# Performance work log

Hardware: AMD Instinct MI355X
Metric: run time of the kernel (lower is better)

## Reference

```python
import jax, jax.numpy as jnp
import numpy as np

B, S, D_MODEL = 2, 2048, 2048
N_HEADS, D_HEAD = 32, 64
SEQ_MAX = 2048


def _rope_cache(seq_len, d_head):
    half = d_head // 2
    inv_freq = 1.0 / (10000.0 ** (np.arange(0, half, dtype=np.float32) / half))
    t = np.arange(seq_len, dtype=np.float32)
    freqs = np.einsum('i,j->ij', t, inv_freq)  # [S, half]
    emb = np.concatenate([freqs, freqs], axis=-1)  # [S, d_head]
    return jnp.asarray(np.cos(emb)), jnp.asarray(np.sin(emb))


def _rotate_half(x):
    half = x.shape[-1] // 2
    return jnp.concatenate([-x[..., half:], x[..., :half]], axis=-1)


def setup_inputs() -> dict:
    key = jax.random.key(0)
    ks = jax.random.split(key, 9)
    std = 0.02
    mk = lambda k: jax.random.normal(k, (D_MODEL, D_MODEL), jnp.float32) * std
    return {
        'x': jax.random.normal(ks[0], (B, S, D_MODEL), jnp.float32),
        'Wq': mk(ks[1]), 'bq': jnp.zeros((D_MODEL,), jnp.float32),
        'Wk': mk(ks[2]), 'bk': jnp.zeros((D_MODEL,), jnp.float32),
        'Wv': mk(ks[3]), 'bv': jnp.zeros((D_MODEL,), jnp.float32),
        'Wo': mk(ks[4]), 'bo': jnp.zeros((D_MODEL,), jnp.float32),
    }


def reference(x, Wq, bq, Wk, bk, Wv, bv, Wo, bo):
    Bsz, S_len, _ = x.shape
    # projections (torch Linear: y = x @ W^T + b)
    q = x @ Wq.T + bq
    k = x @ Wk.T + bk
    v = x @ Wv.T + bv
    # [B, H, S, Dh]
    to_heads = lambda t: t.reshape(Bsz, S_len, N_HEADS, D_HEAD).transpose(0, 2, 1, 3)
    q, k, v = to_heads(q), to_heads(k), to_heads(v)
    cos, sin = _rope_cache(S_len, D_HEAD)  # [S, Dh]
    cos = cos[None, None]
    sin = sin[None, None]
    q = q * cos + _rotate_half(q) * sin
    k = k * cos + _rotate_half(k) * sin
    scale = 1.0 / jnp.sqrt(jnp.float32(D_HEAD))
    att = jnp.einsum('bhqd,bhkd->bhqk', q, k) * scale
    causal = jnp.tril(jnp.ones((S_len, S_len), dtype=bool))
    att = jnp.where(causal[None, None], att, jnp.float32(-jnp.inf))
    att = jax.nn.softmax(att, axis=-1)
    # sigmoid-gated values (dropout = identity at inference)
    y = jnp.einsum('bhqk,bhkd->bhqd', att, jax.nn.sigmoid(v))
    y = y.transpose(0, 2, 1, 3).reshape(Bsz, S_len, D_MODEL)
    return y @ Wo.T + bo
```

## Files before the change

kernel.cpp:

```cpp
#include <hip/hip_runtime.h>

typedef unsigned short u16;
typedef float f32x4 __attribute__((ext_vector_type(4)));
typedef __bf16 bf16x8 __attribute__((ext_vector_type(8)));

#define S_LEN 2048
#define DM 2048
#define NHEAD 32
#define DHEAD 64

__device__ __forceinline__ u16 f2bf(float f) {
    __bf16 b = (__bf16)f;
    return __builtin_bit_cast(u16, b);
}
__device__ __forceinline__ float bf2f(u16 u) {
    return (float)__builtin_bit_cast(__bf16, u);
}
__device__ __forceinline__ void async16(const void* g, void* l) {
    __builtin_amdgcn_global_load_lds(
        (const __attribute__((address_space(1))) unsigned int*)g,
        (__attribute__((address_space(3))) unsigned int*)l, 16, 0, 0);
}
__device__ __forceinline__ void fast_sincos(float th, float* s, float* c) {
    float rev = th * 0.15915494309189535f;
    rev = rev - floorf(rev);
    *s = __builtin_amdgcn_sinf(rev);
    *c = __builtin_amdgcn_cosf(rev);
}
__device__ __forceinline__ float fexp2(float x) { return __builtin_amdgcn_exp2f(x); }

__global__ __launch_bounds__(256) void cast_all(const float* __restrict__ x,
                                                const float* __restrict__ Wq,
                                                const float* __restrict__ Wk,
                                                const float* __restrict__ Wv,
                                                const float* __restrict__ Wo,
                                                u16* __restrict__ xb,
                                                u16* __restrict__ Wqkv,
                                                u16* __restrict__ Wob) {
    int bid = blockIdx.x;
    const float* src;
    u16* dst;
    long long off;
    if (bid < 8192)       { src = x;  dst = xb;             off = (long long)bid * 1024; }
    else if (bid < 12288) { src = Wq; dst = Wqkv;           off = (long long)(bid - 8192) * 1024; }
    else if (bid < 16384) { src = Wk; dst = Wqkv + 4194304; off = (long long)(bid - 12288) * 1024; }
    else if (bid < 20480) { src = Wv; dst = Wqkv + 8388608; off = (long long)(bid - 16384) * 1024; }
    else                  { src = Wo; dst = Wob;            off = (long long)(bid - 20480) * 1024; }
    long long i = off + threadIdx.x * 4;
    float4 f = *(const float4*)(src + i);
    ushort4 v;
    v.x = f2bf(f.x); v.y = f2bf(f.y); v.z = f2bf(f.z); v.w = f2bf(f.w);
    *(ushort4*)(dst + i) = v;
}

__global__ __launch_bounds__(256) void rope_qk(u16* __restrict__ Qb, u16* __restrict__ Kb) {
    long long idx = (long long)blockIdx.x * 256 + threadIdx.x;
    int which = (int)(idx >> 22);
    int t = (int)(idx & 4194303);
    int j = t & 31;
    int h = (t >> 5) & 31;
    int row = t >> 10;
    int s = row & (S_LEN - 1);
    u16* T = which ? Kb : Qb;
    float scale = which ? 1.0f : 0.18033688011112042f;
    long long base = (long long)row * DM + h * DHEAD;
    float inv = __expf(-(float)j * 0.28782313662425575f);
    float sn, cs;
    fast_sincos((float)s * inv, &sn, &cs);
    float x1 = bf2f(T[base + j]);
    float x2 = bf2f(T[base + 32 + j]);
    T[base + j] = f2bf((x1 * cs - x2 * sn) * scale);
    T[base + 32 + j] = f2bf((x2 * cs + x1 * sn) * scale);
}

__global__ __launch_bounds__(256) void gemm_qkv(const u16* __restrict__ A,
                                                const u16* __restrict__ Bt,
                                                const float* __restrict__ bq,
                                                const float* __restrict__ bk,
                                                const float* __restrict__ bv,
                                                u16* __restrict__ Qo, u16* __restrict__ Ko,
                                                u16* __restrict__ VTo, int M, int K) {
    __shared__ __align__(16) u16 As[128 * 32];
    __shared__ __align__(16) u16 Bs[128 * 32];
    int tid = threadIdx.x;
    int w = tid >> 6, lane = tid & 63, quad = lane >> 4, l16 = lane & 15;
    int m0 = blockIdx.x * 128;
    int n0 = blockIdx.y * 128;
    int sel = n0 >> 11;
    int nloc = n0 & 2047;
    int wm = (w & 1) * 64, wn = (w >> 1) * 64;

    f32x4 acc[4][4] = {};
    const u16* ga = A + (long long)m0 * K;
    const u16* gb = Bt + (long long)n0 * K;

    for (int k0 = 0; k0 < K; k0 += 32) {
#pragma unroll
        for (int rr = 0; rr < 2; ++rr) {
            int c = tid + rr * 256;
            int row = c >> 2, kc = c & 3;
            async16(ga + (long long)row * K + k0 + kc * 8, (char*)As + c * 16);
            async16(gb + (long long)row * K + k0 + kc * 8, (char*)Bs + c * 16);
        }
        __syncthreads();
        bf16x8 af[4], bfv[4];
#pragma unroll
        for (int mt = 0; mt < 4; ++mt)
            af[mt] = *(const bf16x8*)(As + (wm + mt * 16 + l16) * 32 + quad * 8);
#pragma unroll
        for (int nt = 0; nt < 4; ++nt)
            bfv[nt] = *(const bf16x8*)(Bs + (wn + nt * 16 + l16) * 32 + quad * 8);
#pragma unroll
        for (int mt = 0; mt < 4; ++mt)
#pragma unroll
            for (int nt = 0; nt < 4; ++nt)
                acc[mt][nt] = __builtin_amdgcn_mfma_f32_16x16x32_bf16(af[mt], bfv[nt],
                                                                      acc[mt][nt], 0, 0, 0);
        __syncthreads();
    }

    if (sel < 2) {
        u16* out = sel == 0 ? Qo : Ko;
        const float* bias = sel == 0 ? bq : bk;
#pragma unroll
        for (int mt = 0; mt < 4; ++mt) {
#pragma unroll
            for (int nt = 0; nt < 4; ++nt) {
                int col = nloc + wn + nt * 16 + l16;
                float bvs = bias[col];
#pragma unroll
                for (int r = 0; r < 4; ++r) {
                    int row = m0 + wm + mt * 16 + quad * 4 + r;
                    out[(long long)row * 2048 + col] = f2bf(acc[mt][nt][r] + bvs);
                }
            }
        }
    } else {
#pragma unroll
        for (int mt = 0; mt < 4; ++mt) {
            int rowb = m0 + wm + mt * 16 + quad * 4;
            int b = rowb >> 11;
            int s0 = rowb & (S_LEN - 1);
#pragma unroll
            for (int nt = 0; nt < 4; ++nt) {
                int col = nloc + wn + nt * 16 + l16;
                int h = col >> 6, d = col & 63;
                float bvs = bv[col];
                ushort4 pk;
                pk.x = f2bf(1.f / (1.f + __expf(-(acc[mt][nt][0] + bvs))));
                pk.y = f2bf(1.f / (1.f + __expf(-(acc[mt][nt][1] + bvs))));
                pk.z = f2bf(1.f / (1.f + __expf(-(acc[mt][nt][2] + bvs))));
                pk.w = f2bf(1.f / (1.f + __expf(-(acc[mt][nt][3] + bvs))));
                *(ushort4*)(VTo + ((long long)((b * NHEAD + h) * DHEAD + d)) * S_LEN + s0) = pk;
            }
        }
    }
}

__global__ __launch_bounds__(256) void gemm_bt_f32(const u16* __restrict__ A,
                                                   const u16* __restrict__ Bt,
                                                   const float* __restrict__ bias,
                                                   float* __restrict__ Cout,
                                                   int M, int N, int K) {
    __shared__ __align__(16) u16 As[128 * 32];
    __shared__ __align__(16) u16 Bs[128 * 32];
    int tid = threadIdx.x;
    int w = tid >> 6, lane = tid & 63, quad = lane >> 4, l16 = lane & 15;
    int m0 = blockIdx.x * 128;
    int n0 = blockIdx.y * 128;
    int wm = (w & 1) * 64, wn = (w >> 1) * 64;

    f32x4 acc[4][4] = {};
    const u16* ga = A + (long long)m0 * K;
    const u16* gb = Bt + (long long)n0 * K;

    for (int k0 = 0; k0 < K; k0 += 32) {
#pragma unroll
        for (int rr = 0; rr < 2; ++rr) {
            int c = tid + rr * 256;
            int row = c >> 2, kc = c & 3;
            async16(ga + (long long)row * K + k0 + kc * 8, (char*)As + c * 16);
            async16(gb + (long long)row * K + k0 + kc * 8, (char*)Bs + c * 16);
        }
        __syncthreads();
        bf16x8 af[4], bfv[4];
#pragma unroll
        for (int mt = 0; mt < 4; ++mt)
            af[mt] = *(const bf16x8*)(As + (wm + mt * 16 + l16) * 32 + quad * 8);
#pragma unroll
        for (int nt = 0; nt < 4; ++nt)
            bfv[nt] = *(const bf16x8*)(Bs + (wn + nt * 16 + l16) * 32 + quad * 8);
#pragma unroll
        for (int mt = 0; mt < 4; ++mt)
#pragma unroll
            for (int nt = 0; nt < 4; ++nt)
                acc[mt][nt] = __builtin_amdgcn_mfma_f32_16x16x32_bf16(af[mt], bfv[nt],
                                                                      acc[mt][nt], 0, 0, 0);
        __syncthreads();
    }

#pragma unroll
    for (int mt = 0; mt < 4; ++mt) {
#pragma unroll
        for (int nt = 0; nt < 4; ++nt) {
            int col = n0 + wn + nt * 16 + l16;
            float bvs = bias[col];
#pragma unroll
            for (int r = 0; r < 4; ++r) {
                int row = m0 + wm + mt * 16 + quad * 4 + r;
                Cout[(long long)row * N + col] = acc[mt][nt][r] + bvs;
            }
        }
    }
}

__global__ __launch_bounds__(256, 2) void flash_attn(const u16* __restrict__ Q,
                                                     const u16* __restrict__ K,
                                                     const u16* __restrict__ VT,
                                                     u16* __restrict__ Y) {
    int bid = blockIdx.x;
    int pi = bid & 7;
    int h = (bid >> 3) & 31;
    int b = bid >> 8;
    int tid = threadIdx.x;
    int w = tid >> 6, lane = tid & 63, quad = lane >> 4, l16 = lane & 15;

    __shared__ __align__(16) u16 Kl[2][64 * 64];
    __shared__ __align__(16) u16 Vl[2][64 * 64];
    __shared__ __align__(16) u16 Pl[4][32 * 64];

    const u16* kbase = K + ((long long)(b * S_LEN)) * DM + h * DHEAD;
    const u16* vbase = VT + ((long long)((b * NHEAD + h) * DHEAD)) * S_LEN;

    bf16x8 kpre[2], vpre[2];
    int c0 = tid, c1 = tid + 256;
    int row0 = c0 >> 3, lc0 = (c0 & 7) ^ (row0 & 7);
    int row1 = c1 >> 3, lc1 = (c1 & 7) ^ (row1 & 7);

    kpre[0] = *(const bf16x8*)(kbase + (long long)row0 * DM + lc0 * 8);
    vpre[0] = *(const bf16x8*)(vbase + (long long)row0 * S_LEN + lc0 * 8);
    kpre[1] = *(const bf16x8*)(kbase + (long long)row1 * DM + lc1 * 8);
    vpre[1] = *(const bf16x8*)(vbase + (long long)row1 * S_LEN + lc1 * 8);

    int it = 0;
#pragma unroll 1
    for (int rep = 0; rep < 2; ++rep) {
        int qt = rep ? 15 - pi : pi;
        bf16x8 aq[2][2];
#pragma unroll
        for (int sub = 0; sub < 2; ++sub) {
            int qrow = qt * 128 + w * 32 + sub * 16 + l16;
            const u16* qp = Q + ((long long)(b * S_LEN + qrow)) * DM + h * DHEAD + quad * 8;
            aq[sub][0] = *(const bf16x8*)(qp);
            aq[sub][1] = *(const bf16x8*)(qp + 32);
        }

        f32x4 o[2][4] = {};
        float m_r[2] = {-__builtin_inff(), -__builtin_inff()};
        float l_r[2] = {0.f, 0.f};

        int kts = 2 * qt + 2;
#pragma unroll 1
        for (int kt = 0; kt < kts; ++kt) {
            u16* Kb_ = Kl[it & 1];
            u16* Vb_ = Vl[it & 1];
            *(bf16x8*)((char*)Kb_ + c0 * 16) = kpre[0];
            *(bf16x8*)((char*)Vb_ + c0 * 16) = vpre[0];
            *(bf16x8*)((char*)Kb_ + c1 * 16) = kpre[1];
            *(bf16x8*)((char*)Vb_ + c1 * 16) = vpre[1];
            {
                int nk0 = (kt + 1 < kts ? kt + 1 : 0) * 64;
                kpre[0] = *(const bf16x8*)(kbase + (long long)(nk0 + row0) * DM + lc0 * 8);
                vpre[0] = *(const bf16x8*)(vbase + (long long)row0 * S_LEN + nk0 + lc0 * 8);
                kpre[1] = *(const bf16x8*)(kbase + (long long)(nk0 + row1) * DM + lc1 * 8);
                vpre[1] = *(const bf16x8*)(vbase + (long long)row1 * S_LEN + nk0 + lc1 * 8);
            }
            __syncthreads();

            bf16x8 ak0[4], ak1[4];
#pragma unroll
            for (int nt = 0; nt < 4; ++nt) {
                int row = nt * 16 + l16;
                ak0[nt] = *(const bf16x8*)(Kb_ + row * 64 + (quad ^ (row & 7)) * 8);
                ak1[nt] = *(const bf16x8*)(Kb_ + row * 64 + ((quad + 4) ^ (row & 7)) * 8);
            }

            bf16x8 bp[2][2];
            u16* pw = &Pl[w][0];
#pragma unroll
            for (int sub = 0; sub < 2; ++sub) {
                f32x4 s[4];
#pragma unroll
                for (int nt = 0; nt < 4; ++nt) {
                    f32x4 a = {};
                    a = __builtin_amdgcn_mfma_f32_16x16x32_bf16(ak0[nt], aq[sub][0], a, 0, 0, 0);
                    a = __builtin_amdgcn_mfma_f32_16x16x32_bf16(ak1[nt], aq[sub][1], a, 0, 0, 0);
                    s[nt] = a;
                }
                if (kt >= 2 * qt) {
                    int qg = qt * 128 + w * 32 + sub * 16 + l16;
#pragma unroll
                    for (int nt = 0; nt < 4; ++nt) {
#pragma unroll
                        for (int r = 0; r < 4; ++r) {
                            int kg = kt * 64 + nt * 16 + quad * 4 + r;
                            if (kg > qg) s[nt][r] = -__builtin_inff();
                        }
                    }
                }
                float mx = s[0][0];
#pragma unroll
                for (int nt = 0; nt < 4; ++nt)
#pragma unroll
                    for (int r = 0; r < 4; ++r) mx = fmaxf(mx, s[nt][r]);
                mx = fmaxf(mx, __shfl_xor(mx, 16, 64));
                mx = fmaxf(mx, __shfl_xor(mx, 32, 64));
                float mnew = fmaxf(m_r[sub], mx);
                float alpha = fexp2(m_r[sub] - mnew);
                m_r[sub] = mnew;
#pragma unroll
                for (int nt = 0; nt < 4; ++nt)
#pragma unroll
                    for (int r = 0; r < 4; ++r) s[nt][r] = fexp2(s[nt][r] - mnew);
                float sum = 0.f;
#pragma unroll
                for (int nt = 0; nt < 4; ++nt)
#pragma unroll
                    for (int r = 0; r < 4; ++r) sum += s[nt][r];
                sum += __shfl_xor(sum, 16, 64);
                sum += __shfl_xor(sum, 32, 64);
                l_r[sub] = l_r[sub] * alpha + sum;
#pragma unroll
                for (int dt = 0; dt < 4; ++dt)
#pragma unroll
                    for (int r = 0; r < 4; ++r) o[sub][dt][r] *= alpha;

                int prow = sub * 16 + l16;
#pragma unroll
                for (int nt = 0; nt < 4; ++nt) {
                    ushort4 pk;
                    pk.x = f2bf(s[nt][0]); pk.y = f2bf(s[nt][1]);
                    pk.z = f2bf(s[nt][2]); pk.w = f2bf(s[nt][3]);
                    int chunk = (nt * 2 + (quad >> 1)) ^ (l16 & 7);
                    *(ushort4*)(pw + prow * 64 + chunk * 8 + (quad & 1) * 4) = pk;
                }
                bp[sub][0] = *(const bf16x8*)(pw + prow * 64 + (quad ^ (l16 & 7)) * 8);
                bp[sub][1] = *(const bf16x8*)(pw + prow * 64 + ((quad + 4) ^ (l16 & 7)) * 8);
            }

#pragma unroll
            for (int dt = 0; dt < 4; ++dt) {
                int row = dt * 16 + l16;
                bf16x8 av0 = *(const bf16x8*)(Vb_ + row * 64 + (quad ^ (row & 7)) * 8);
                bf16x8 av1 = *(const bf16x8*)(Vb_ + row * 64 + ((quad + 4) ^ (row & 7)) * 8);
#pragma unroll
                for (int sub = 0; sub < 2; ++sub) {
                    o[sub][dt] = __builtin_amdgcn_mfma_f32_16x16x32_bf16(av0, bp[sub][0],
                                                                         o[sub][dt], 0, 0, 0);
                    o[sub][dt] = __builtin_amdgcn_mfma_f32_16x16x32_bf16(av1, bp[sub][1],
                                                                         o[sub][dt], 0, 0, 0);
                }
            }
            ++it;
        }

#pragma unroll
        for (int sub = 0; sub < 2; ++sub) {
            float inv_l = 1.f / l_r[sub];
            u16* yp = Y + ((long long)(b * S_LEN + qt * 128 + w * 32 + sub * 16 + l16)) * DM
                      + h * DHEAD;
#pragma unroll
            for (int dt = 0; dt < 4; ++dt) {
                ushort4 yk;
                yk.x = f2bf(o[sub][dt][0] * inv_l);
                yk.y = f2bf(o[sub][dt][1] * inv_l);
                yk.z = f2bf(o[sub][dt][2] * inv_l);
                yk.w = f2bf(o[sub][dt][3] * inv_l);
                *(ushort4*)(yp + dt * 16 + quad * 4) = yk;
            }
        }
    }
}

extern "C" void kernel_launch(void* const* d_in, const int* in_sizes, int n_in,
                              void* d_out, int out_size, void* d_ws, size_t ws_size,
                              hipStream_t stream) {
    const float* x  = (const float*)d_in[0];
    const float* Wq = (const float*)d_in[1];
    const float* bq = (const float*)d_in[2];
    const float* Wk = (const float*)d_in[3];
    const float* bk = (const float*)d_in[4];
    const float* Wv = (const float*)d_in[5];
    const float* bv = (const float*)d_in[6];
    const float* Wo = (const float*)d_in[7];
    const float* bo = (const float*)d_in[8];

    const long long M = 2LL * S_LEN;

    char* ws = (char*)d_ws;
    u16* xb   = (u16*)(ws);
    u16* Wqkv = (u16*)(ws + 16 * 1024 * 1024);
    u16* Wob  = (u16*)(ws + 40 * 1024 * 1024);
    u16* Qb   = (u16*)(ws + 48 * 1024 * 1024);
    u16* Kb   = (u16*)(ws + 64 * 1024 * 1024);
    u16* VTb  = (u16*)(ws + 80 * 1024 * 1024);
    u16* Yb   = (u16*)(ws + 96 * 1024 * 1024);

    cast_all<<<24576, 256, 0, stream>>>(x, Wq, Wk, Wv, Wo, xb, Wqkv, Wob);

    dim3 gqkv(32, 48);
    gemm_qkv<<<gqkv, 256, 0, stream>>>(xb, Wqkv, bq, bk, bv, Qb, Kb, VTb, (int)M, DM);

    rope_qk<<<32768, 256, 0, stream>>>(Qb, Kb);

    flash_attn<<<2 * NHEAD * 8, 256, 0, stream>>>(Qb, Kb, VTb, Yb);

    dim3 gg(32, 16);
    gemm_bt_f32<<<gg, 256, 0, stream>>>(Yb, Wob, bo, (float*)d_out, (int)M, DM, DM);
}
```

Before: 431.1 us.

## Move V sigmoid and transpose into RoPE kernel; remap attention blocks per XCD

The QKV GEMM epilogue no longer writes V with a strided, scattered transpose. It now writes V row-major like Q and K, and a new branch in the RoPE kernel applies the sigmoid and transposes 64x64 tiles through shared memory into the VT layout. The flash attention block index is also remapped so that blocks sharing a head land on the same XCD, which should improve L2 reuse of K and V. The cost is an extra write and read pass over V plus a larger workspace.

```diff
diff --git a/kernel.cpp b/kernel.cpp
--- a/kernel.cpp
+++ b/kernel.cpp
@@ -53,24 +53,53 @@
     *(ushort4*)(dst + i) = v;
 }
 
-__global__ __launch_bounds__(256) void rope_qk(u16* __restrict__ Qb, u16* __restrict__ Kb) {
-    long long idx = (long long)blockIdx.x * 256 + threadIdx.x;
-    int which = (int)(idx >> 22);
-    int t = (int)(idx & 4194303);
-    int j = t & 31;
-    int h = (t >> 5) & 31;
-    int row = t >> 10;
-    int s = row & (S_LEN - 1);
-    u16* T = which ? Kb : Qb;
-    float scale = which ? 1.0f : 0.18033688011112042f;
-    long long base = (long long)row * DM + h * DHEAD;
-    float inv = __expf(-(float)j * 0.28782313662425575f);
-    float sn, cs;
-    fast_sincos((float)s * inv, &sn, &cs);
-    float x1 = bf2f(T[base + j]);
-    float x2 = bf2f(T[base + 32 + j]);
-    T[base + j] = f2bf((x1 * cs - x2 * sn) * scale);
-    T[base + 32 + j] = f2bf((x2 * cs + x1 * sn) * scale);
+__global__ __launch_bounds__(256) void rope_vsig(u16* __restrict__ Qb, u16* __restrict__ Kb,
+                                                 const u16* __restrict__ V,
+                                                 u16* __restrict__ VT) {
+    int bid = blockIdx.x;
+    if (bid < 32768) {
+        long long idx = (long long)bid * 256 + threadIdx.x;
+        int which = (int)(idx >> 22);
+        int t = (int)(idx & 4194303);
+        int j = t & 31;
+        int h = (t >> 5) & 31;
+        int row = t >> 10;
+        int s = row & (S_LEN - 1);
+        u16* T = which ? Kb : Qb;
+        float scale = which ? 1.0f : 0.18033688011112042f;
+        long long base = (long long)row * DM + h * DHEAD;
+        float inv = __expf(-(float)j * 0.28782313662425575f);
+        float sn, cs;
+        fast_sincos((float)s * inv, &sn, &cs);
+        float x1 = bf2f(T[base + j]);
+        float x2 = bf2f(T[base + 32 + j]);
+        T[base + j] = f2bf((x1 * cs - x2 * sn) * scale);
+        T[base + 32 + j] = f2bf((x2 * cs + x1 * sn) * scale);
+    } else {
+        int vb = bid - 32768;
+        int st = vb & 63;
+        int h = vb >> 6;
+        __shared__ u16 T[64][72];
+        int r = threadIdx.x >> 2, c0 = (threadIdx.x & 3) * 16;
+        const u16* src = V + (long long)(st * 64 + r) * DM + h * 64 + c0;
+#pragma unroll
+        for (int half = 0; half < 2; ++half) {
+            bf16x8 v = *(const bf16x8*)(src + half * 8);
+#pragma unroll
+            for (int j = 0; j < 8; ++j) {
+                float vf = (float)v[j];
+                T[c0 + half * 8 + j][r] = f2bf(1.f / (1.f + __expf(-vf)));
+            }
+        }
+        __syncthreads();
+        int d = threadIdx.x >> 2, s0 = (threadIdx.x & 3) * 16;
+        int b = st >> 5;
+        int sl = (st & 31) * 64;
+        u16* dst = VT + ((long long)((b * NHEAD + h) * DHEAD + d)) * S_LEN + sl + s0;
+#pragma unroll
+        for (int q = 0; q < 4; ++q)
+            *(ushort4*)(dst + q * 4) = *(const ushort4*)(&T[d][s0] + q * 4);
+    }
 }
 
 __global__ __launch_bounds__(256) void gemm_qkv(const u16* __restrict__ A,
@@ -79,7 +108,7 @@
                                                 const float* __restrict__ bk,
                                                 const float* __restrict__ bv,
                                                 u16* __restrict__ Qo, u16* __restrict__ Ko,
-                                                u16* __restrict__ VTo, int M, int K) {
+                                                u16* __restrict__ Vo, int M, int K) {
     __shared__ __align__(16) u16 As[128 * 32];
     __shared__ __align__(16) u16 Bs[128 * 32];
     int tid = threadIdx.x;
@@ -88,6 +117,8 @@
     int n0 = blockIdx.y * 128;
     int sel = n0 >> 11;
     int nloc = n0 & 2047;
+    u16* out = sel == 0 ? Qo : (sel == 1 ? Ko : Vo);
+    const float* bias = sel == 0 ? bq : (sel == 1 ? bk : bv);
     int wm = (w & 1) * 64, wn = (w >> 1) * 64;
 
     f32x4 acc[4][4] = {};
@@ -119,39 +150,16 @@
         __syncthreads();
     }
 
-    if (sel < 2) {
-        u16* out = sel == 0 ? Qo : Ko;
-        const float* bias = sel == 0 ? bq : bk;
-#pragma unroll
-        for (int mt = 0; mt < 4; ++mt) {
-#pragma unroll
-            for (int nt = 0; nt < 4; ++nt) {
-                int col = nloc + wn + nt * 16 + l16;
-                float bvs = bias[col];
-#pragma unroll
-                for (int r = 0; r < 4; ++r) {
-                    int row = m0 + wm + mt * 16 + quad * 4 + r;
-                    out[(long long)row * 2048 + col] = f2bf(acc[mt][nt][r] + bvs);
-                }
-            }
-        }
-    } else {
-#pragma unroll
-        for (int mt = 0; mt < 4; ++mt) {
-            int rowb = m0 + wm + mt * 16 + quad * 4;
-            int b = rowb >> 11;
-            int s0 = rowb & (S_LEN - 1);
-#pragma unroll
-            for (int nt = 0; nt < 4; ++nt) {
-                int col = nloc + wn + nt * 16 + l16;
-                int h = col >> 6, d = col & 63;
-                float bvs = bv[col];
-                ushort4 pk;
-                pk.x = f2bf(1.f / (1.f + __expf(-(acc[mt][nt][0] + bvs))));
-                pk.y = f2bf(1.f / (1.f + __expf(-(acc[mt][nt][1] + bvs))));
-                pk.z = f2bf(1.f / (1.f + __expf(-(acc[mt][nt][2] + bvs))));
-                pk.w = f2bf(1.f / (1.f + __expf(-(acc[mt][nt][3] + bvs))));
-                *(ushort4*)(VTo + ((long long)((b * NHEAD + h) * DHEAD + d)) * S_LEN + s0) = pk;
+#pragma unroll
+    for (int mt = 0; mt < 4; ++mt) {
+#pragma unroll
+        for (int nt = 0; nt < 4; ++nt) {
+            int col = nloc + wn + nt * 16 + l16;
+            float bvs = bias[col];
+#pragma unroll
+            for (int r = 0; r < 4; ++r) {
+                int row = m0 + wm + mt * 16 + quad * 4 + r;
+                out[(long long)row * 2048 + col] = f2bf(acc[mt][nt][r] + bvs);
             }
         }
     }
@@ -219,9 +227,11 @@
                                                      const u16* __restrict__ VT,
                                                      u16* __restrict__ Y) {
     int bid = blockIdx.x;
-    int pi = bid & 7;
-    int h = (bid >> 3) & 31;
-    int b = bid >> 8;
+    int xcd = bid & 7;
+    int idx = bid >> 3;
+    int pi = idx & 7;
+    int hg = xcd * 8 + (idx >> 3);
+    int b = hg >> 5, h = hg & 31;
     int tid = threadIdx.x;
     int w = tid >> 6, lane = tid & 63, quad = lane >> 4, l16 = lane & 15;
 
@@ -403,15 +413,16 @@
     u16* Wob  = (u16*)(ws + 40 * 1024 * 1024);
     u16* Qb   = (u16*)(ws + 48 * 1024 * 1024);
     u16* Kb   = (u16*)(ws + 64 * 1024 * 1024);
-    u16* VTb  = (u16*)(ws + 80 * 1024 * 1024);
+    u16* Vb   = (u16*)(ws + 80 * 1024 * 1024);
     u16* Yb   = (u16*)(ws + 96 * 1024 * 1024);
+    u16* VTb  = (u16*)(ws + 112 * 1024 * 1024);
 
     cast_all<<<24576, 256, 0, stream>>>(x, Wq, Wk, Wv, Wo, xb, Wqkv, Wob);
 
     dim3 gqkv(32, 48);
-    gemm_qkv<<<gqkv, 256, 0, stream>>>(xb, Wqkv, bq, bk, bv, Qb, Kb, VTb, (int)M, DM);
-
-    rope_qk<<<32768, 256, 0, stream>>>(Qb, Kb);
+    gemm_qkv<<<gqkv, 256, 0, stream>>>(xb, Wqkv, bq, bk, bv, Qb, Kb, Vb, (int)M, DM);
+
+    rope_vsig<<<34816, 256, 0, stream>>>(Qb, Kb, Vb, VTb);
 
     flash_attn<<<2 * NHEAD * 8, 256, 0, stream>>>(Qb, Kb, VTb, Yb);
 
```

After: 415.2 us. 3.7% less time.
